# Kernel optimization log

Measured on AMD Instinct MI355X. Metric: run time of the kernel, lower is better.

The kernel has to match this reference:

```python
import jax, jax.numpy as jnp
import numpy as np

B, D_IN, D_H = 262144, 64, 128


def setup_inputs() -> dict:
    key = jax.random.key(0)
    ks = jax.random.split(key, 15)
    mk = lambda k, shape: jax.random.normal(k, shape, dtype=jnp.float32) * 0.05
    return {
        "x": mk(ks[0], (B, D_IN)),
        "prev_hidden": mk(ks[1], (B, D_H)),
        "prev_memory": mk(ks[2], (B, D_H)),
        "Wi_w": mk(ks[3], (D_H, D_IN)), "Wi_b": mk(ks[4], (D_H,)),
        "Vi_w": mk(ks[5], (D_H, D_H)),  "Vi_b": mk(ks[6], (D_H,)),
        "Wf_w": mk(ks[7], (D_H, D_IN)), "Wf_b": mk(ks[8], (D_H,)),
        "Vf_w": mk(ks[9], (D_H, D_H)),  "Vf_b": mk(ks[10], (D_H,)),
        "Wo_w": mk(ks[11], (D_H, D_IN)), "Wo_b": mk(ks[12], (D_H,)),
        "Vo_w": mk(ks[13], (D_H, D_H)),  "Vo_b": mk(ks[14], (D_H,)),
    }


def _lin(x, w, b):
    # nn.Linear: x @ w.T + b
    return jnp.einsum('bi,oi->bo', x, w) + b


def reference(x, prev_hidden, prev_memory,
              Wi_w, Wi_b, Vi_w, Vi_b,
              Wf_w, Wf_b, Vf_w, Vf_b,
              Wo_w, Wo_b, Vo_w, Vo_b):
    sig = jax.nn.sigmoid
    wi_x = _lin(x, Wi_w, Wi_b)  # reused for both I and C (quirk of source)
    I = sig(wi_x + _lin(prev_hidden, Vi_w, Vi_b))
    F = sig(_lin(x, Wf_w, Wf_b) + _lin(prev_hidden, Vf_w, Vf_b))
    O = sig(_lin(x, Wo_w, Wo_b) + _lin(prev_hidden, Vo_w, Vo_b))
    # source uses Wi/Vi (not Wc/Vc) and sigmoid for the candidate, on F*prev_hidden
    C = sig(wi_x + _lin(F * prev_hidden, Vi_w, Vi_b))
    Ct = F * prev_memory + I * C
    current_hidden = O * jnp.tanh(Ct)
    return (Ct, current_hidden)
```

## Files before the change

kernel.cpp:

```cpp
#include <hip/hip_runtime.h>
#include <hip/hip_bf16.h>

typedef __bf16 bf8 __attribute__((ext_vector_type(8)));
typedef float  f4  __attribute__((ext_vector_type(4)));

#define RT 64
#define MS 4

__device__ __forceinline__ float fsig(float v) {
    return __builtin_amdgcn_rcpf(1.0f + __expf(-v));
}

__device__ __forceinline__ bf8 cvt8(f4 a, f4 b) {
    bf8 r;
    r[0] = (__bf16)a[0]; r[1] = (__bf16)a[1]; r[2] = (__bf16)a[2]; r[3] = (__bf16)a[3];
    r[4] = (__bf16)b[0]; r[5] = (__bf16)b[1]; r[6] = (__bf16)b[2]; r[7] = (__bf16)b[3];
    return r;
}

__device__ __forceinline__ unsigned pk2(float a, float b) {
    union { __bf16 h; unsigned short s; } ua, ub;
    ua.h = (__bf16)a; ub.h = (__bf16)b;
    return ((unsigned)ub.s << 16) | (unsigned)ua.s;
}
__device__ __forceinline__ float upk(unsigned v, int hi) {
    union { unsigned short s; __bf16 h; } u;
    u.s = (unsigned short)(hi ? (v >> 16) : (v & 0xffffu));
    return (float)u.h;
}

__global__ void pack_weights(
    const float* __restrict__ Wi, const float* __restrict__ Vi,
    const float* __restrict__ Wf, const float* __restrict__ Vf,
    const float* __restrict__ Wo, const float* __restrict__ Vo,
    const float* __restrict__ Wib, const float* __restrict__ Vib,
    const float* __restrict__ Wfb, const float* __restrict__ Vfb,
    const float* __restrict__ Wob, const float* __restrict__ Vob,
    __bf16* __restrict__ wsW, float* __restrict__ wsB)
{
    const int t = blockIdx.x * 256 + threadIdx.x;
    if (t < 73728) {
        const int fg   = t >> 9;
        const int l8   = t & 511;
        const int lane = l8 >> 3, j = l8 & 7;
        const int w    = fg / 18, f = fg % 18;
        const int nrow = w * 16 + (lane & 15);
        const int kq   = (lane >> 4) << 3;
        float v;
        if (f < 6) {
            const float* M = (f < 2) ? Wi : (f < 4) ? Wf : Wo;
            v = M[nrow * 64 + (f & 1) * 32 + kq + j];
        } else {
            const int f2 = f - 6;
            const float* M = (f2 < 4) ? Vi : (f2 < 8) ? Vf : Vo;
            v = M[nrow * 128 + (f2 & 3) * 32 + kq + j];
        }
        wsW[t] = (__bf16)v;
    } else if (t < 74112) {
        const int c = t - 73728;
        const int col = c & 127, m = c >> 7;
        wsB[c] = (m == 0) ? Wib[col] + Vib[col]
               : (m == 1) ? Wfb[col] + Vfb[col]
                          : Wob[col] + Vob[col];
    }
}

__global__ __launch_bounds__(512, 2) void lstm_main(
    const float* __restrict__ x, const float* __restrict__ h,
    const float* __restrict__ mem,
    const bf8* __restrict__ wsW, const float* __restrict__ wsB,
    float* __restrict__ out, long long Bn)
{
    __shared__ __align__(16) __bf16 smX[RT * 64];
    __shared__ __align__(16) __bf16 smH[RT * 128];
    __shared__ __align__(16) __bf16 smG[RT * 128 + 64];

    const int tid  = threadIdx.x;
    const int lane = tid & 63;
    const int wv   = tid >> 6;
    const int nrow = wv * 16 + (lane & 15);
    const int kq   = (lane >> 4) << 3;
    const long long b0 = (long long)blockIdx.x * RT;

    const bf8* wbase = wsW + (size_t)wv * 18 * 64 + lane;

    {
        const int rowx = tid >> 3, kbx = tid & 7;
        const float* px = x + (size_t)(b0 + rowx) * 64 + kbx * 8;
        *(bf8*)&smX[rowx * 64 + ((kbx * 8) ^ ((rowx & 7) << 3))] =
            cvt8(*(const f4*)px, *(const f4*)(px + 4));
#pragma unroll
        for (int ph = 0; ph < 2; ++ph) {
            const int task = tid + ph * 512;
            const int rowh = task >> 4, kbh = task & 15;
            const float* q = h + (size_t)(b0 + rowh) * 128 + kbh * 8;
            *(bf8*)&smH[rowh * 128 + ((kbh * 8) ^ ((rowh & 7) << 3))] =
                cvt8(*(const f4*)q, *(const f4*)(q + 4));
        }
    }

    bf8 Wf0 = wbase[2 * 64],  Wf1 = wbase[3 * 64];
    bf8 Vf0 = wbase[10 * 64], Vf1 = wbase[11 * 64];
    bf8 Vf2 = wbase[12 * 64], Vf3 = wbase[13 * 64];
    const float bF = wsB[128 + nrow];
    __syncthreads();

    unsigned FP[MS][2];
#pragma unroll
    for (int ms = 0; ms < MS; ++ms) {
        const int rA = ms * 16 + (lane & 15);
        f4 pf = {0.f, 0.f, 0.f, 0.f};
        {
            bf8 a0 = *(const bf8*)&smX[rA * 64 + ((0 * 32 + kq) ^ ((rA & 7) << 3))];
            bf8 a1 = *(const bf8*)&smX[rA * 64 + ((1 * 32 + kq) ^ ((rA & 7) << 3))];
            pf = __builtin_amdgcn_mfma_f32_16x16x32_bf16(a0, Wf0, pf, 0, 0, 0);
            pf = __builtin_amdgcn_mfma_f32_16x16x32_bf16(a1, Wf1, pf, 0, 0, 0);
        }
        {
            bf8 a0 = *(const bf8*)&smH[rA * 128 + ((0 * 32 + kq) ^ ((rA & 7) << 3))];
            bf8 a1 = *(const bf8*)&smH[rA * 128 + ((1 * 32 + kq) ^ ((rA & 7) << 3))];
            bf8 a2 = *(const bf8*)&smH[rA * 128 + ((2 * 32 + kq) ^ ((rA & 7) << 3))];
            bf8 a3 = *(const bf8*)&smH[rA * 128 + ((3 * 32 + kq) ^ ((rA & 7) << 3))];
            pf = __builtin_amdgcn_mfma_f32_16x16x32_bf16(a0, Vf0, pf, 0, 0, 0);
            pf = __builtin_amdgcn_mfma_f32_16x16x32_bf16(a1, Vf1, pf, 0, 0, 0);
            pf = __builtin_amdgcn_mfma_f32_16x16x32_bf16(a2, Vf2, pf, 0, 0, 0);
            pf = __builtin_amdgcn_mfma_f32_16x16x32_bf16(a3, Vf3, pf, 0, 0, 0);
        }
        float fv[4];
#pragma unroll
        for (int i = 0; i < 4; ++i) {
            const float Fi  = fsig(pf[i] + bF);
            const int   row = ms * 16 + ((lane >> 4) << 2) + i;
            const int   e   = row * 128 + (nrow ^ ((row & 7) << 3));
            smG[e] = (__bf16)(Fi * (float)smH[e]);
            fv[i]  = Fi;
        }
        FP[ms][0] = pk2(fv[0], fv[1]);
        FP[ms][1] = pk2(fv[2], fv[3]);
    }
    __syncthreads();
    __builtin_amdgcn_sched_barrier(0);

    bf8 Wo0 = wbase[4 * 64],  Wo1 = wbase[5 * 64];
    bf8 Vo0 = wbase[14 * 64], Vo1 = wbase[15 * 64];
    bf8 Vo2 = wbase[16 * 64], Vo3 = wbase[17 * 64];
    const float bO = wsB[256 + nrow];
    unsigned OP[MS][2];
#pragma unroll
    for (int ms = 0; ms < MS; ++ms) {
        const int rA = ms * 16 + (lane & 15);
        f4 po = {0.f, 0.f, 0.f, 0.f};
        {
            bf8 a0 = *(const bf8*)&smX[rA * 64 + ((0 * 32 + kq) ^ ((rA & 7) << 3))];
            bf8 a1 = *(const bf8*)&smX[rA * 64 + ((1 * 32 + kq) ^ ((rA & 7) << 3))];
            po = __builtin_amdgcn_mfma_f32_16x16x32_bf16(a0, Wo0, po, 0, 0, 0);
            po = __builtin_amdgcn_mfma_f32_16x16x32_bf16(a1, Wo1, po, 0, 0, 0);
        }
        {
            bf8 a0 = *(const bf8*)&smH[rA * 128 + ((0 * 32 + kq) ^ ((rA & 7) << 3))];
            bf8 a1 = *(const bf8*)&smH[rA * 128 + ((1 * 32 + kq) ^ ((rA & 7) << 3))];
            bf8 a2 = *(const bf8*)&smH[rA * 128 + ((2 * 32 + kq) ^ ((rA & 7) << 3))];
            bf8 a3 = *(const bf8*)&smH[rA * 128 + ((3 * 32 + kq) ^ ((rA & 7) << 3))];
            po = __builtin_amdgcn_mfma_f32_16x16x32_bf16(a0, Vo0, po, 0, 0, 0);
            po = __builtin_amdgcn_mfma_f32_16x16x32_bf16(a1, Vo1, po, 0, 0, 0);
            po = __builtin_amdgcn_mfma_f32_16x16x32_bf16(a2, Vo2, po, 0, 0, 0);
            po = __builtin_amdgcn_mfma_f32_16x16x32_bf16(a3, Vo3, po, 0, 0, 0);
        }
        OP[ms][0] = pk2(fsig(po[0] + bO), fsig(po[1] + bO));
        OP[ms][1] = pk2(fsig(po[2] + bO), fsig(po[3] + bO));
    }
    __builtin_amdgcn_sched_barrier(0);

    bf8 Wi0 = wbase[0],      Wi1 = wbase[64];
    bf8 Vi0 = wbase[6 * 64], Vi1 = wbase[7 * 64];
    bf8 Vi2 = wbase[8 * 64], Vi3 = wbase[9 * 64];
    const float bI = wsB[nrow];
    const size_t outH = (size_t)Bn * 128;

#pragma unroll
    for (int ms = 0; ms < MS; ++ms) {
        const int rA = ms * 16 + (lane & 15);
        f4 memv;
#pragma unroll
        for (int i = 0; i < 4; ++i) {
            const int row = ms * 16 + ((lane >> 4) << 2) + i;
            memv[i] = mem[(size_t)(b0 + row) * 128 + nrow];
        }
        f4 wix = {0.f, 0.f, 0.f, 0.f};
        {
            bf8 a0 = *(const bf8*)&smX[rA * 64 + ((0 * 32 + kq) ^ ((rA & 7) << 3))];
            bf8 a1 = *(const bf8*)&smX[rA * 64 + ((1 * 32 + kq) ^ ((rA & 7) << 3))];
            wix = __builtin_amdgcn_mfma_f32_16x16x32_bf16(a0, Wi0, wix, 0, 0, 0);
            wix = __builtin_amdgcn_mfma_f32_16x16x32_bf16(a1, Wi1, wix, 0, 0, 0);
        }
        f4 aI = wix, aC = wix;
        {
            bf8 a0 = *(const bf8*)&smH[rA * 128 + ((0 * 32 + kq) ^ ((rA & 7) << 3))];
            bf8 a1 = *(const bf8*)&smH[rA * 128 + ((1 * 32 + kq) ^ ((rA & 7) << 3))];
            bf8 a2 = *(const bf8*)&smH[rA * 128 + ((2 * 32 + kq) ^ ((rA & 7) << 3))];
            bf8 a3 = *(const bf8*)&smH[rA * 128 + ((3 * 32 + kq) ^ ((rA & 7) << 3))];
            aI = __builtin_amdgcn_mfma_f32_16x16x32_bf16(a0, Vi0, aI, 0, 0, 0);
            aI = __builtin_amdgcn_mfma_f32_16x16x32_bf16(a1, Vi1, aI, 0, 0, 0);
            aI = __builtin_amdgcn_mfma_f32_16x16x32_bf16(a2, Vi2, aI, 0, 0, 0);
            aI = __builtin_amdgcn_mfma_f32_16x16x32_bf16(a3, Vi3, aI, 0, 0, 0);
        }
        {
            bf8 g0 = *(const bf8*)&smG[rA * 128 + ((0 * 32 + kq) ^ ((rA & 7) << 3))];
            bf8 g1 = *(const bf8*)&smG[rA * 128 + ((1 * 32 + kq) ^ ((rA & 7) << 3))];
            bf8 g2 = *(const bf8*)&smG[rA * 128 + ((2 * 32 + kq) ^ ((rA & 7) << 3))];
            bf8 g3 = *(const bf8*)&smG[rA * 128 + ((3 * 32 + kq) ^ ((rA & 7) << 3))];
            aC = __builtin_amdgcn_mfma_f32_16x16x32_bf16(g0, Vi0, aC, 0, 0, 0);
            aC = __builtin_amdgcn_mfma_f32_16x16x32_bf16(g1, Vi1, aC, 0, 0, 0);
            aC = __builtin_amdgcn_mfma_f32_16x16x32_bf16(g2, Vi2, aC, 0, 0, 0);
            aC = __builtin_amdgcn_mfma_f32_16x16x32_bf16(g3, Vi3, aC, 0, 0, 0);
        }
#pragma unroll
        for (int i = 0; i < 4; ++i) {
            const float Iv = fsig(aI[i] + bI);
            const float Cv = fsig(aC[i] + bI);
            const float Fi = upk(FP[ms][i >> 1], i & 1);
            const float Ov = upk(OP[ms][i >> 1], i & 1);
            const float ct = Fi * memv[i] + Iv * Cv;
            const float e2 = __expf(2.0f * ct);
            const float th = 1.0f - 2.0f * __builtin_amdgcn_rcpf(e2 + 1.0f);
            const int   row = ms * 16 + ((lane >> 4) << 2) + i;
            const size_t g  = (size_t)(b0 + row) * 128 + nrow;
            out[g]        = ct;
            out[outH + g] = Ov * th;
        }
    }
}

extern "C" void kernel_launch(void* const* d_in, const int* in_sizes, int n_in,
                              void* d_out, int out_size, void* d_ws, size_t ws_size,
                              hipStream_t stream) {
    const float* x   = (const float*)d_in[0];
    const float* h   = (const float*)d_in[1];
    const float* mem = (const float*)d_in[2];
    const float* Wi  = (const float*)d_in[3];
    const float* Wib = (const float*)d_in[4];
    const float* Vi  = (const float*)d_in[5];
    const float* Vib = (const float*)d_in[6];
    const float* Wf  = (const float*)d_in[7];
    const float* Wfb = (const float*)d_in[8];
    const float* Vf  = (const float*)d_in[9];
    const float* Vfb = (const float*)d_in[10];
    const float* Wo  = (const float*)d_in[11];
    const float* Wob = (const float*)d_in[12];
    const float* Vo  = (const float*)d_in[13];
    const float* Vob = (const float*)d_in[14];
    float* out = (float*)d_out;

    __bf16* wsW = (__bf16*)d_ws;
    float*  wsB = (float*)((char*)d_ws + 147456);

    pack_weights<<<290, 256, 0, stream>>>(Wi, Vi, Wf, Vf, Wo, Vo,
                                          Wib, Vib, Wfb, Vfb, Wob, Vob, wsW, wsB);

    const long long Bn = (long long)(in_sizes[1] / 128);
    const int blocks = (int)(Bn / RT);

    lstm_main<<<blocks, 512, 0, stream>>>(x, h, mem, (const bf8*)wsW, wsB, out, Bn);
}
```

Baseline: 163.5 us.

## Double row tile, fuse F and O gate passes, prefetch memory ahead

Doubles the rows per block from 64 to 128, so each block stages twice as much x and h in shared memory. The F and O gate matmuls now run interleaved in one pass over the same A fragments, which removes a separate loop, its shared-memory reloads and a barrier. prev_memory loads are software-pipelined three row tiles ahead of use. The cost is about 80 KB of LDS per block, which may stop two blocks from fitting per CU at the declared launch bounds, plus more live registers and half as many blocks in the grid.

```diff
diff --git a/kernel.cpp b/kernel.cpp
--- a/kernel.cpp
+++ b/kernel.cpp
@@ -4,8 +4,8 @@
 typedef __bf16 bf8 __attribute__((ext_vector_type(8)));
 typedef float  f4  __attribute__((ext_vector_type(4)));
 
-#define RT 64
-#define MS 4
+#define RT 128
+#define MS 8
 
 __device__ __forceinline__ float fsig(float v) {
     return __builtin_amdgcn_rcpf(1.0f + __expf(-v));
@@ -73,7 +73,7 @@
 {
     __shared__ __align__(16) __bf16 smX[RT * 64];
     __shared__ __align__(16) __bf16 smH[RT * 128];
-    __shared__ __align__(16) __bf16 smG[RT * 128 + 64];
+    __shared__ __align__(16) __bf16 smG[RT * 128];
 
     const int tid  = threadIdx.x;
     const int lane = tid & 63;
@@ -85,12 +85,16 @@
     const bf8* wbase = wsW + (size_t)wv * 18 * 64 + lane;
 
     {
-        const int rowx = tid >> 3, kbx = tid & 7;
-        const float* px = x + (size_t)(b0 + rowx) * 64 + kbx * 8;
-        *(bf8*)&smX[rowx * 64 + ((kbx * 8) ^ ((rowx & 7) << 3))] =
-            cvt8(*(const f4*)px, *(const f4*)(px + 4));
 #pragma unroll
         for (int ph = 0; ph < 2; ++ph) {
+            const int task = tid + ph * 512;
+            const int rowx = task >> 3, kbx = task & 7;
+            const float* px = x + (size_t)(b0 + rowx) * 64 + kbx * 8;
+            *(bf8*)&smX[rowx * 64 + ((kbx * 8) ^ ((rowx & 7) << 3))] =
+                cvt8(*(const f4*)px, *(const f4*)(px + 4));
+        }
+#pragma unroll
+        for (int ph = 0; ph < 4; ++ph) {
             const int task = tid + ph * 512;
             const int rowh = task >> 4, kbh = task & 15;
             const float* q = h + (size_t)(b0 + rowh) * 128 + kbh * 8;
@@ -102,19 +106,27 @@
     bf8 Wf0 = wbase[2 * 64],  Wf1 = wbase[3 * 64];
     bf8 Vf0 = wbase[10 * 64], Vf1 = wbase[11 * 64];
     bf8 Vf2 = wbase[12 * 64], Vf3 = wbase[13 * 64];
+    bf8 Wo0 = wbase[4 * 64],  Wo1 = wbase[5 * 64];
+    bf8 Vo0 = wbase[14 * 64], Vo1 = wbase[15 * 64];
+    bf8 Vo2 = wbase[16 * 64], Vo3 = wbase[17 * 64];
     const float bF = wsB[128 + nrow];
+    const float bO = wsB[256 + nrow];
     __syncthreads();
 
     unsigned FP[MS][2];
+    unsigned OP[MS][2];
 #pragma unroll
     for (int ms = 0; ms < MS; ++ms) {
         const int rA = ms * 16 + (lane & 15);
         f4 pf = {0.f, 0.f, 0.f, 0.f};
+        f4 po = {0.f, 0.f, 0.f, 0.f};
         {
             bf8 a0 = *(const bf8*)&smX[rA * 64 + ((0 * 32 + kq) ^ ((rA & 7) << 3))];
             bf8 a1 = *(const bf8*)&smX[rA * 64 + ((1 * 32 + kq) ^ ((rA & 7) << 3))];
             pf = __builtin_amdgcn_mfma_f32_16x16x32_bf16(a0, Wf0, pf, 0, 0, 0);
+            po = __builtin_amdgcn_mfma_f32_16x16x32_bf16(a0, Wo0, po, 0, 0, 0);
             pf = __builtin_amdgcn_mfma_f32_16x16x32_bf16(a1, Wf1, pf, 0, 0, 0);
+            po = __builtin_amdgcn_mfma_f32_16x16x32_bf16(a1, Wo1, po, 0, 0, 0);
         }
         {
             bf8 a0 = *(const bf8*)&smH[rA * 128 + ((0 * 32 + kq) ^ ((rA & 7) << 3))];
@@ -122,9 +134,13 @@
             bf8 a2 = *(const bf8*)&smH[rA * 128 + ((2 * 32 + kq) ^ ((rA & 7) << 3))];
             bf8 a3 = *(const bf8*)&smH[rA * 128 + ((3 * 32 + kq) ^ ((rA & 7) << 3))];
             pf = __builtin_amdgcn_mfma_f32_16x16x32_bf16(a0, Vf0, pf, 0, 0, 0);
+            po = __builtin_amdgcn_mfma_f32_16x16x32_bf16(a0, Vo0, po, 0, 0, 0);
             pf = __builtin_amdgcn_mfma_f32_16x16x32_bf16(a1, Vf1, pf, 0, 0, 0);
+            po = __builtin_amdgcn_mfma_f32_16x16x32_bf16(a1, Vo1, po, 0, 0, 0);
             pf = __builtin_amdgcn_mfma_f32_16x16x32_bf16(a2, Vf2, pf, 0, 0, 0);
+            po = __builtin_amdgcn_mfma_f32_16x16x32_bf16(a2, Vo2, po, 0, 0, 0);
             pf = __builtin_amdgcn_mfma_f32_16x16x32_bf16(a3, Vf3, pf, 0, 0, 0);
+            po = __builtin_amdgcn_mfma_f32_16x16x32_bf16(a3, Vo3, po, 0, 0, 0);
         }
         float fv[4];
 #pragma unroll
@@ -137,38 +153,10 @@
         }
         FP[ms][0] = pk2(fv[0], fv[1]);
         FP[ms][1] = pk2(fv[2], fv[3]);
-    }
-    __syncthreads();
-    __builtin_amdgcn_sched_barrier(0);
-
-    bf8 Wo0 = wbase[4 * 64],  Wo1 = wbase[5 * 64];
-    bf8 Vo0 = wbase[14 * 64], Vo1 = wbase[15 * 64];
-    bf8 Vo2 = wbase[16 * 64], Vo3 = wbase[17 * 64];
-    const float bO = wsB[256 + nrow];
-    unsigned OP[MS][2];
-#pragma unroll
-    for (int ms = 0; ms < MS; ++ms) {
-        const int rA = ms * 16 + (lane & 15);
-        f4 po = {0.f, 0.f, 0.f, 0.f};
-        {
-            bf8 a0 = *(const bf8*)&smX[rA * 64 + ((0 * 32 + kq) ^ ((rA & 7) << 3))];
-            bf8 a1 = *(const bf8*)&smX[rA * 64 + ((1 * 32 + kq) ^ ((rA & 7) << 3))];
-            po = __builtin_amdgcn_mfma_f32_16x16x32_bf16(a0, Wo0, po, 0, 0, 0);
-            po = __builtin_amdgcn_mfma_f32_16x16x32_bf16(a1, Wo1, po, 0, 0, 0);
-        }
-        {
-            bf8 a0 = *(const bf8*)&smH[rA * 128 + ((0 * 32 + kq) ^ ((rA & 7) << 3))];
-            bf8 a1 = *(const bf8*)&smH[rA * 128 + ((1 * 32 + kq) ^ ((rA & 7) << 3))];
-            bf8 a2 = *(const bf8*)&smH[rA * 128 + ((2 * 32 + kq) ^ ((rA & 7) << 3))];
-            bf8 a3 = *(const bf8*)&smH[rA * 128 + ((3 * 32 + kq) ^ ((rA & 7) << 3))];
-            po = __builtin_amdgcn_mfma_f32_16x16x32_bf16(a0, Vo0, po, 0, 0, 0);
-            po = __builtin_amdgcn_mfma_f32_16x16x32_bf16(a1, Vo1, po, 0, 0, 0);
-            po = __builtin_amdgcn_mfma_f32_16x16x32_bf16(a2, Vo2, po, 0, 0, 0);
-            po = __builtin_amdgcn_mfma_f32_16x16x32_bf16(a3, Vo3, po, 0, 0, 0);
-        }
         OP[ms][0] = pk2(fsig(po[0] + bO), fsig(po[1] + bO));
         OP[ms][1] = pk2(fsig(po[2] + bO), fsig(po[3] + bO));
     }
+    __syncthreads();
     __builtin_amdgcn_sched_barrier(0);
 
     bf8 Wi0 = wbase[0],      Wi1 = wbase[64];
@@ -177,15 +165,24 @@
     const float bI = wsB[nrow];
     const size_t outH = (size_t)Bn * 128;
 
-#pragma unroll
-    for (int ms = 0; ms < MS; ++ms) {
-        const int rA = ms * 16 + (lane & 15);
-        f4 memv;
+    auto ldmem = [&](int ms) -> f4 {
+        f4 r;
 #pragma unroll
         for (int i = 0; i < 4; ++i) {
             const int row = ms * 16 + ((lane >> 4) << 2) + i;
-            memv[i] = mem[(size_t)(b0 + row) * 128 + nrow];
-        }
+            r[i] = mem[(size_t)(b0 + row) * 128 + nrow];
+        }
+        return r;
+    };
+    f4 mv[4];
+    mv[0] = ldmem(0);
+    mv[1] = ldmem(1);
+    mv[2] = ldmem(2);
+
+#pragma unroll
+    for (int ms = 0; ms < MS; ++ms) {
+        if (ms + 3 < MS) mv[(ms + 3) & 3] = ldmem(ms + 3);
+        const int rA = ms * 16 + (lane & 15);
         f4 wix = {0.f, 0.f, 0.f, 0.f};
         {
             bf8 a0 = *(const bf8*)&smX[rA * 64 + ((0 * 32 + kq) ^ ((rA & 7) << 3))];
@@ -220,7 +217,7 @@
             const float Cv = fsig(aC[i] + bI);
             const float Fi = upk(FP[ms][i >> 1], i & 1);
             const float Ov = upk(OP[ms][i >> 1], i & 1);
-            const float ct = Fi * memv[i] + Iv * Cv;
+            const float ct = Fi * mv[ms & 3][i] + Iv * Cv;
             const float e2 = __expf(2.0f * ct);
             const float th = 1.0f - 2.0f * __builtin_amdgcn_rcpf(e2 + 1.0f);
             const int   row = ms * 16 + ((lane >> 4) << 2) + i;
```

After: 167.1 us. +2.2%, slower.
